# Optimization experiments

Hardware: AMD Instinct MI355X
Metric: run time of the kernel (lower is better)

## Reference

```python
import jax, jax.numpy as jnp
import numpy as np

B, S, E, H = 2, 2048, 1024, 16
D = E // H


def setup_inputs() -> dict:
    key = jax.random.key(0)
    ks = jax.random.split(key, 8)
    q = jax.random.normal(ks[0], (B, S, E), dtype=jnp.float32)
    k = jax.random.normal(ks[1], (B, S, E), dtype=jnp.float32)
    v = jax.random.normal(ks[2], (B, S, E), dtype=jnp.float32)
    mask = jax.random.randint(ks[3], (B, 1, 1, S), 0, 2, dtype=jnp.int32)
    sc = 1.0 / np.sqrt(E)
    W_qkv = jax.random.normal(ks[4], (3 * E, E), dtype=jnp.float32) * sc
    b_qkv = jnp.zeros((3 * E,), dtype=jnp.float32)
    W_out = jax.random.normal(ks[5], (E, E), dtype=jnp.float32) * sc
    b_out = jnp.zeros((E,), dtype=jnp.float32)
    return {"q": q, "k": k, "v": v, "mask": mask,
            "W_qkv": W_qkv, "b_qkv": b_qkv, "W_out": W_out, "b_out": b_out}


def reference(q, k, v, mask, W_qkv, b_qkv, W_out, b_out):
    # Fused qkv linear: q takes the Q-slice, k the K-slice, v the V-slice.
    qp = (q @ W_qkv[:E].T + b_qkv[:E]).reshape(B, S, H, D)
    kp = (k @ W_qkv[E:2 * E].T + b_qkv[E:2 * E]).reshape(B, S, H, D)
    vp = (v @ W_qkv[2 * E:].T + b_qkv[2 * E:]).reshape(B, S, H, D)
    # (B,H,S,S) scores -- NOTE: original module does NOT scale by sqrt(d)
    energy = jnp.einsum('nqhd,nkhd->nhqk', qp, kp)
    energy = jnp.where(mask == 0, jnp.float32(-1e20), energy)
    attention = jax.nn.softmax(energy, axis=-1)
    out = jnp.einsum('nhql,nlhd->nqhd', attention, vp).reshape(B, S, E)
    return out @ W_out.T + b_out
```

## Files before the change

kernel.cpp:

```cpp
#include <hip/hip_runtime.h>
#include <stdint.h>

constexpr int B_ = 2, S_ = 2048, E_ = 1024, H_ = 16, D_ = 64;
constexpr int M_ = B_ * S_;

typedef unsigned short u16;
typedef __attribute__((ext_vector_type(8))) short short8;
typedef __attribute__((ext_vector_type(4))) float f32x4;

__device__ __forceinline__ u16 f2bf(float f) {
  uint32_t u = __float_as_uint(f);
  return (u16)((u + 0x7FFFu + ((u >> 16) & 1u)) >> 16);
}
__device__ __forceinline__ void tsplit(float x, u16& hi, u16& lo) {
  const uint32_t u = __float_as_uint(x);
  hi = (u16)(u >> 16);
  const float hif = __uint_as_float(u & 0xFFFF0000u);
  lo = (u16)(__float_as_uint(x - hif) >> 16);
}

__device__ __forceinline__ void block_sync() {
  asm volatile("s_waitcnt lgkmcnt(0)" ::: "memory");
  __builtin_amdgcn_s_barrier();
}

__global__ __launch_bounds__(256) void split_f32_kernel(
    const float* __restrict__ src, u16* __restrict__ hi, u16* __restrict__ lo, int n4)
{
  const int i = blockIdx.x * 256 + threadIdx.x;
  if (i >= n4) return;
  const float4 x = ((const float4*)src)[i];
  ushort4 h, l;
  tsplit(x.x, h.x, l.x); tsplit(x.y, h.y, l.y);
  tsplit(x.z, h.z, l.z); tsplit(x.w, h.w, l.w);
  ((ushort4*)hi)[i] = h;
  ((ushort4*)lo)[i] = l;
}

__global__ __launch_bounds__(256) void mask_scan_kernel(
    const int* __restrict__ mask, int* __restrict__ opos, int* __restrict__ nk)
{
  __shared__ int tmp[256];
  __shared__ int coff;
  const int b = blockIdx.x, t = threadIdx.x;
  for (int c = t; c < S_; c += 256) opos[b * S_ + c] = 0;
  if (t == 0) coff = 0;
  __syncthreads();
  for (int c = 0; c < S_; c += 256) {
    const int m = (mask[b * S_ + c + t] != 0) ? 1 : 0;
    int x = m;
    tmp[t] = x;
    __syncthreads();
#pragma unroll
    for (int off = 1; off < 256; off <<= 1) {
      const int v = (t >= off) ? tmp[t - off] : 0;
      __syncthreads();
      x += v;
      tmp[t] = x;
      __syncthreads();
    }
    const int base = coff;
    if (m) opos[b * S_ + base + x - 1] = c + t;
    __syncthreads();
    if (t == 255) coff = base + x;
    __syncthreads();
  }
  if (t == 0) nk[b] = coff;
}

__global__ __launch_bounds__(256) void gemm_qkv_kernel(
    const float* __restrict__ q, const float* __restrict__ k, const float* __restrict__ v,
    const u16* __restrict__ WHi, const u16* __restrict__ WLo,
    const float* __restrict__ bias,
    const int* __restrict__ Opos, const int* __restrict__ NkArr,
    u16* __restrict__ QpHi, u16* __restrict__ QpLo,
    u16* __restrict__ KpHi, u16* __restrict__ KpLo,
    u16* __restrict__ Vp)
{
  __shared__ __align__(16) short smem[20480];
  short* Ah = smem;
  short* Al = smem + 5120;
  short* Bh = smem + 10240;
  short* Bl = smem + 15360;

  const int t = threadIdx.x;
  const int m0 = blockIdx.x * 128;
  const int n0g = blockIdx.y * 128;
  const int proj = n0g >> 10;
  const int nloc = n0g & (E_ - 1);
  const bool split = (proj < 2);
  const int bb = m0 >> 11, mloc = m0 & (S_ - 1);
  const int nkb = NkArr[bb];
  if (proj != 0 && mloc >= nkb) return;

  const float* A = (proj == 0) ? q : (proj == 1) ? k : v;

  const int w = t >> 6, lane = t & 63;
  const int g = lane >> 4, lc = lane & 15;
  const int wm = w & 1, wn = w >> 1;
  const int srow = t >> 1, sh = (t & 1) * 16;

  int arow;
  if (proj == 0) arow = m0 + srow;
  else arow = bb * S_ + (Opos[bb * S_ + mloc + srow] & (S_ - 1));
  const float* Ab = A + (size_t)arow * E_ + sh;
  const u16* Bhb = WHi + (size_t)(n0g + srow) * E_ + sh;
  const u16* Blb = WLo + (size_t)(n0g + srow) * E_ + sh;

  f32x4 acc[4][4];
#pragma unroll
  for (int i = 0; i < 4; ++i)
#pragma unroll
    for (int j = 0; j < 4; ++j) acc[i][j] = (f32x4){0.f, 0.f, 0.f, 0.f};

  float4 ar[4]; short8 br[2], cr[2];
#pragma unroll
  for (int i = 0; i < 4; ++i) ar[i] = *(const float4*)(Ab + 4 * i);
  br[0] = *(const short8*)(Bhb);     br[1] = *(const short8*)(Bhb + 8);
  if (split) { cr[0] = *(const short8*)(Blb); cr[1] = *(const short8*)(Blb + 8); }

  for (int k0 = 0; k0 < E_; k0 += 32) {
    __syncthreads();
    {
      ushort hh[16], ll[16];
#pragma unroll
      for (int i = 0; i < 4; ++i) {
        tsplit(ar[i].x, hh[4 * i + 0], ll[4 * i + 0]);
        tsplit(ar[i].y, hh[4 * i + 1], ll[4 * i + 1]);
        tsplit(ar[i].z, hh[4 * i + 2], ll[4 * i + 2]);
        tsplit(ar[i].w, hh[4 * i + 3], ll[4 * i + 3]);
      }
      *(short8*)&Ah[srow * 40 + sh]     = *(const short8*)&hh[0];
      *(short8*)&Ah[srow * 40 + sh + 8] = *(const short8*)&hh[8];
      if (split) {
        *(short8*)&Al[srow * 40 + sh]     = *(const short8*)&ll[0];
        *(short8*)&Al[srow * 40 + sh + 8] = *(const short8*)&ll[8];
      }
    }
    *(short8*)&Bh[srow * 40 + sh]     = br[0];
    *(short8*)&Bh[srow * 40 + sh + 8] = br[1];
    if (split) {
      *(short8*)&Bl[srow * 40 + sh]     = cr[0];
      *(short8*)&Bl[srow * 40 + sh + 8] = cr[1];
    }
    __syncthreads();
    if (k0 + 32 < E_) {
#pragma unroll
      for (int i = 0; i < 4; ++i) ar[i] = *(const float4*)(Ab + k0 + 32 + 4 * i);
      br[0] = *(const short8*)(Bhb + k0 + 32); br[1] = *(const short8*)(Bhb + k0 + 40);
      if (split) {
        cr[0] = *(const short8*)(Blb + k0 + 32); cr[1] = *(const short8*)(Blb + k0 + 40);
      }
    }

    short8 ah[4], al[4], bh[4], bl[4];
#pragma unroll
    for (int mt = 0; mt < 4; ++mt) {
      const int ro = (wm * 64 + mt * 16 + lc) * 40 + g * 8;
      ah[mt] = *(const short8*)&Ah[ro];
      if (split) al[mt] = *(const short8*)&Al[ro];
    }
#pragma unroll
    for (int nt = 0; nt < 4; ++nt) {
      const int ro = (wn * 64 + nt * 16 + lc) * 40 + g * 8;
      bh[nt] = *(const short8*)&Bh[ro];
      if (split) bl[nt] = *(const short8*)&Bl[ro];
    }
#pragma unroll
    for (int mt = 0; mt < 4; ++mt)
#pragma unroll
      for (int nt = 0; nt < 4; ++nt) {
        f32x4 a = acc[mt][nt];
        a = __builtin_amdgcn_mfma_f32_16x16x32_bf16(ah[mt], bh[nt], a, 0, 0, 0);
        if (split) {
          a = __builtin_amdgcn_mfma_f32_16x16x32_bf16(ah[mt], bl[nt], a, 0, 0, 0);
          a = __builtin_amdgcn_mfma_f32_16x16x32_bf16(al[mt], bh[nt], a, 0, 0, 0);
        }
        acc[mt][nt] = a;
      }
  }

  float bs[4];
#pragma unroll
  for (int nt = 0; nt < 4; ++nt) bs[nt] = bias[n0g + wn * 64 + nt * 16 + lc];

  if (proj < 2) {
    u16* Hi = (proj == 0) ? QpHi : KpHi;
    u16* Lo = (proj == 0) ? QpLo : KpLo;
    const int hwave = (nloc + wn * 64) >> 6;
    short* T = smem + w * 4608;
    const int srow_out = (proj == 0) ? ((m0 + wm * 64 + lane) & (S_ - 1))
                                     : (mloc + wm * 64 + lane);
    const size_t rowb = (((size_t)(bb * H_ + hwave)) * S_ + srow_out) * D_;
#pragma unroll
    for (int pass = 0; pass < 2; ++pass) {
      __syncthreads();
#pragma unroll
      for (int nt = 0; nt < 4; ++nt)
#pragma unroll
        for (int mt = 0; mt < 4; ++mt)
#pragma unroll
          for (int r = 0; r < 4; ++r) {
            const float val = acc[mt][nt][r] + bs[nt];
            const uint32_t u = __float_as_uint(val);
            u16 x;
            if (pass == 0) x = (u16)(u >> 16);
            else {
              const float hif = __uint_as_float(u & 0xFFFF0000u);
              x = (u16)(__float_as_uint(val - hif) >> 16);
            }
            T[(mt * 16 + g * 4 + r) * 72 + nt * 16 + lc] = (short)x;
          }
      __syncthreads();
      u16* dst = (pass == 0) ? Hi : Lo;
#pragma unroll
      for (int j = 0; j < 8; ++j)
        *(short8*)&dst[rowb + 8 * j] = *(const short8*)&T[lane * 72 + 8 * j];
    }
  } else {
#pragma unroll
    for (int mt = 0; mt < 4; ++mt) {
      const int jb = mloc + wm * 64 + mt * 16 + g * 4;
#pragma unroll
      for (int nt = 0; nt < 4; ++nt) {
        const int nE = nloc + wn * 64 + nt * 16 + lc;
        const int h = nE >> 6, d = nE & 63;
        const size_t rb = (((size_t)(bb * H_ + h)) * D_ + d) * S_;
#pragma unroll
        for (int r = 0; r < 4; ++r) {
          if (jb + r < nkb) Vp[rb + jb + r] = f2bf(acc[mt][nt][r] + bs[nt]);
        }
      }
    }
  }
}

__global__ __launch_bounds__(256, 4) void attn_mfma_kernel(
    const u16* __restrict__ QpHi, const u16* __restrict__ QpLo,
    const u16* __restrict__ KpHi, const u16* __restrict__ KpLo,
    const u16* __restrict__ Vp,
    const int* __restrict__ nkArr,
    u16* __restrict__ AOHi)
{
  __shared__ __align__(16) short sm[18432];
  short* Khi = sm;
  short* Klo = sm + 4608;
  short* Vt  = sm + 9216;
  short* Pb  = sm + 13824;

  const int t = threadIdx.x;
  const int w = t >> 6, lane = t & 63;
  const int g = lane >> 4, lc = lane & 15;
  const int bh = blockIdx.y;
  const int b = bh >> 4, hh = bh & 15;
  const int q0 = blockIdx.x * 64;
  const size_t hb = (size_t)bh * S_ * D_;
  const u16* QgH = QpHi + hb;
  const u16* QgL = QpLo + hb;
  const u16* KgH = KpHi + hb;
  const u16* KgL = KpLo + hb;
  const u16* Vg  = Vp + hb;
  short* Pw = Pb + w * 1152;

  const int nk = nkArr[b];
  const int kend = ((nk + 63) >> 6) << 6;

  short8 qh[2], ql[2];
  {
    const size_t base = (size_t)(q0 + 16 * w + lc) * D_ + 8 * g;
    qh[0] = *(const short8*)&QgH[base];
    qh[1] = *(const short8*)&QgH[base + 32];
    ql[0] = *(const short8*)&QgL[base];
    ql[1] = *(const short8*)&QgL[base + 32];
  }

  short8 ones8 = {0, 0, 0, 0, 0, 0, 0, 0};
  if (lc == 0) {
    const short o = (short)0x3F80;
    ones8 = (short8){o, o, o, o, o, o, o, o};
  }

  f32x4 O[4];
  f32x4 Ol = (f32x4){0.f, 0.f, 0.f, 0.f};
#pragma unroll
  for (int dt = 0; dt < 4; ++dt) O[dt] = (f32x4){0.f, 0.f, 0.f, 0.f};
  float mst[4] = {-INFINITY, -INFINITY, -INFINITY, -INFINITY};

  const int srow = t >> 2, sc16 = (t & 3) * 16;

  short8 kr[2], lr[2], vr[2];
  kr[0] = *(const short8*)&KgH[srow * D_ + sc16];
  kr[1] = *(const short8*)&KgH[srow * D_ + sc16 + 8];
  lr[0] = *(const short8*)&KgL[srow * D_ + sc16];
  lr[1] = *(const short8*)&KgL[srow * D_ + sc16 + 8];
  vr[0] = *(const short8*)&Vg[srow * S_ + sc16];
  vr[1] = *(const short8*)&Vg[srow * S_ + sc16 + 8];

  for (int kt = 0; kt < kend; kt += 64) {
    block_sync();
    *(short8*)&Khi[srow * 72 + sc16]     = kr[0];
    *(short8*)&Khi[srow * 72 + sc16 + 8] = kr[1];
    *(short8*)&Klo[srow * 72 + sc16]     = lr[0];
    *(short8*)&Klo[srow * 72 + sc16 + 8] = lr[1];
    *(short8*)&Vt[srow * 72 + sc16]      = vr[0];
    *(short8*)&Vt[srow * 72 + sc16 + 8]  = vr[1];
    block_sync();
    if (kt + 64 < kend) {
      const int kn = kt + 64;
      kr[0] = *(const short8*)&KgH[(kn + srow) * D_ + sc16];
      kr[1] = *(const short8*)&KgH[(kn + srow) * D_ + sc16 + 8];
      lr[0] = *(const short8*)&KgL[(kn + srow) * D_ + sc16];
      lr[1] = *(const short8*)&KgL[(kn + srow) * D_ + sc16 + 8];
      vr[0] = *(const short8*)&Vg[srow * S_ + kn + sc16];
      vr[1] = *(const short8*)&Vg[srow * S_ + kn + sc16 + 8];
    }

    f32x4 sc[4];
#pragma unroll
    for (int kt16 = 0; kt16 < 4; ++kt16) {
      const int ko = (16 * kt16 + lc) * 72 + 8 * g;
      const short8 kh0 = *(const short8*)&Khi[ko];
      const short8 kh1 = *(const short8*)&Khi[ko + 32];
      const short8 kl0 = *(const short8*)&Klo[ko];
      const short8 kl1 = *(const short8*)&Klo[ko + 32];
      f32x4 a = {0.f, 0.f, 0.f, 0.f};
      a = __builtin_amdgcn_mfma_f32_16x16x32_bf16(qh[0], kh0, a, 0, 0, 0);
      a = __builtin_amdgcn_mfma_f32_16x16x32_bf16(qh[1], kh1, a, 0, 0, 0);
      a = __builtin_amdgcn_mfma_f32_16x16x32_bf16(qh[0], kl0, a, 0, 0, 0);
      a = __builtin_amdgcn_mfma_f32_16x16x32_bf16(qh[1], kl1, a, 0, 0, 0);
      a = __builtin_amdgcn_mfma_f32_16x16x32_bf16(ql[0], kh0, a, 0, 0, 0);
      a = __builtin_amdgcn_mfma_f32_16x16x32_bf16(ql[1], kh1, a, 0, 0, 0);
      sc[kt16] = a;
    }

    if (kt + 64 > nk) {
#pragma unroll
      for (int kt16 = 0; kt16 < 4; ++kt16) {
        if (kt + 16 * kt16 + lc >= nk) {
          sc[kt16][0] = -1e20f; sc[kt16][1] = -1e20f;
          sc[kt16][2] = -1e20f; sc[kt16][3] = -1e20f;
        }
      }
    }

    float al[4];
#pragma unroll
    for (int r = 0; r < 4; ++r) {
      float vv = fmaxf(fmaxf(sc[0][r], sc[1][r]), fmaxf(sc[2][r], sc[3][r]));
      vv = fmaxf(vv, __shfl_xor(vv, 1));
      vv = fmaxf(vv, __shfl_xor(vv, 2));
      vv = fmaxf(vv, __shfl_xor(vv, 4));
      vv = fmaxf(vv, __shfl_xor(vv, 8));
      const float mn = fmaxf(mst[r], vv);
      al[r] = __expf(mst[r] - mn);
      mst[r] = mn;
    }
#pragma unroll
    for (int kt16 = 0; kt16 < 4; ++kt16) {
#pragma unroll
      for (int r = 0; r < 4; ++r)
        sc[kt16][r] = __expf(sc[kt16][r] - mst[r]);
    }
    const f32x4 alv = {al[0], al[1], al[2], al[3]};
    O[0] *= alv; O[1] *= alv; O[2] *= alv; O[3] *= alv;
    Ol *= alv;
#pragma unroll
    for (int kt16 = 0; kt16 < 4; ++kt16) {
#pragma unroll
      for (int r = 0; r < 4; ++r)
        Pw[(4 * g + r) * 72 + 16 * kt16 + lc] = (short)f2bf(sc[kt16][r]);
    }

    short8 pa[2];
    pa[0] = *(const short8*)&Pw[lc * 72 + 8 * g];
    pa[1] = *(const short8*)&Pw[lc * 72 + 32 + 8 * g];
    Ol = __builtin_amdgcn_mfma_f32_16x16x32_bf16(pa[0], ones8, Ol, 0, 0, 0);
    Ol = __builtin_amdgcn_mfma_f32_16x16x32_bf16(pa[1], ones8, Ol, 0, 0, 0);
#pragma unroll
    for (int dt = 0; dt < 4; ++dt) {
      const int vo = (16 * dt + lc) * 72 + 8 * g;
      const short8 vb0 = *(const short8*)&Vt[vo];
      const short8 vb1 = *(const short8*)&Vt[vo + 32];
      O[dt] = __builtin_amdgcn_mfma_f32_16x16x32_bf16(pa[0], vb0, O[dt], 0, 0, 0);
      O[dt] = __builtin_amdgcn_mfma_f32_16x16x32_bf16(pa[1], vb1, O[dt], 0, 0, 0);
    }
  }

#pragma unroll
  for (int r = 0; r < 4; ++r) {
    const float lv = __shfl(Ol[r], lane & 48);
    const float lir = 1.0f / lv;
    const int qrow = q0 + 16 * w + 4 * g + r;
    const size_t rowb = (size_t)(b * S_ + qrow) * E_ + hh * 64;
#pragma unroll
    for (int dt = 0; dt < 4; ++dt)
      AOHi[rowb + dt * 16 + lc] = f2bf(O[dt][r] * lir);
  }
}

__global__ __launch_bounds__(256) void gemm_out_kernel(
    const u16* __restrict__ AHi,
    const u16* __restrict__ WHi,
    const float* __restrict__ bias, float* __restrict__ out)
{
  __shared__ __align__(16) short smem[5120];
  short* Ah = smem;
  short* Bh = smem + 2560;

  const int t = threadIdx.x;
  const int m0 = blockIdx.x * 64;
  const int n0 = blockIdx.y * 64;
  const int w = t >> 6, lane = t & 63;
  const int g = lane >> 4, lc = lane & 15;
  const int wm = w & 1, wn = w >> 1;
  const int sr = t >> 2, sc = (t & 3) * 8;

  const u16* Ahb = AHi + (size_t)(m0 + sr) * E_ + sc;
  const u16* Bhb = WHi + (size_t)(n0 + sr) * E_ + sc;

  f32x4 acc[2][2];
#pragma unroll
  for (int i = 0; i < 2; ++i)
#pragma unroll
    for (int j = 0; j < 2; ++j) acc[i][j] = (f32x4){0.f, 0.f, 0.f, 0.f};

  short8 arP[2], brP[2];
  arP[0] = *(const short8*)(Ahb);
  arP[1] = *(const short8*)(Ahb + 32);
  brP[0] = *(const short8*)(Bhb);
  brP[1] = *(const short8*)(Bhb + 32);

#pragma unroll 2
  for (int k0 = 0; k0 < E_; k0 += 32) {
    const int p = (k0 >> 5) & 1;
    block_sync();
    *(short8*)&Ah[sr * 40 + sc] = arP[p];
    *(short8*)&Bh[sr * 40 + sc] = brP[p];
    block_sync();
    {
      const int kk = (k0 + 64) & (E_ - 1);
      arP[p] = *(const short8*)(Ahb + kk);
      brP[p] = *(const short8*)(Bhb + kk);
    }

    short8 ah[2], bh[2];
#pragma unroll
    for (int mt = 0; mt < 2; ++mt)
      ah[mt] = *(const short8*)&Ah[(wm * 32 + mt * 16 + lc) * 40 + g * 8];
#pragma unroll
    for (int nt = 0; nt < 2; ++nt)
      bh[nt] = *(const short8*)&Bh[(wn * 32 + nt * 16 + lc) * 40 + g * 8];
#pragma unroll
    for (int mt = 0; mt < 2; ++mt)
#pragma unroll
      for (int nt = 0; nt < 2; ++nt)
        acc[mt][nt] = __builtin_amdgcn_mfma_f32_16x16x32_bf16(ah[mt], bh[nt], acc[mt][nt], 0, 0, 0);
  }

  float bs[2];
#pragma unroll
  for (int nt = 0; nt < 2; ++nt) bs[nt] = bias[n0 + wn * 32 + nt * 16 + lc];
#pragma unroll
  for (int nt = 0; nt < 2; ++nt) {
    const int nc = n0 + wn * 32 + nt * 16 + lc;
#pragma unroll
    for (int mt = 0; mt < 2; ++mt) {
#pragma unroll
      for (int r = 0; r < 4; ++r) {
        const int mrow = m0 + wm * 32 + mt * 16 + g * 4 + r;
        out[(size_t)mrow * E_ + nc] = acc[mt][nt][r] + bs[nt];
      }
    }
  }
}

extern "C" void kernel_launch(void* const* d_in, const int* in_sizes, int n_in,
                              void* d_out, int out_size, void* d_ws, size_t ws_size,
                              hipStream_t stream) {
  const float* q    = (const float*)d_in[0];
  const float* k    = (const float*)d_in[1];
  const float* v    = (const float*)d_in[2];
  const int*   mask = (const int*)d_in[3];
  const float* Wqkv = (const float*)d_in[4];
  const float* bqkv = (const float*)d_in[5];
  const float* Wout = (const float*)d_in[6];
  const float* bout = (const float*)d_in[7];
  float* out = (float*)d_out;

  char* wsb = (char*)d_ws;
  u16* WqkvHi = (u16*)(wsb + 0);
  u16* WqkvLo = (u16*)(wsb + 6291456);
  u16* WoutHi = (u16*)(wsb + 12582912);
  int* Opos   = (int*)(wsb + 14680064);
  int* Nk     = (int*)(wsb + 14680064 + 16384);
  u16* WoutLo = (u16*)(wsb + 14680064);
  u16* QpHi   = (u16*)(wsb + 16777216);
  u16* QpLo   = (u16*)(wsb + 25165824);
  u16* KpHi   = (u16*)(wsb + 33554432);
  u16* KpLo   = (u16*)(wsb + 41943040);
  u16* Vp     = (u16*)(wsb + 50331648);
  u16* AOHi   = (u16*)(wsb + 58720256);

  hipLaunchKernelGGL(split_f32_kernel, dim3(3072), dim3(256), 0, stream,
                     Wqkv, WqkvHi, WqkvLo, 786432);
  hipLaunchKernelGGL(split_f32_kernel, dim3(1024), dim3(256), 0, stream,
                     Wout, WoutHi, WoutLo, 262144);
  hipLaunchKernelGGL(mask_scan_kernel, dim3(B_), dim3(256), 0, stream,
                     mask, Opos, Nk);
  hipMemsetAsync(Vp, 0, 8388608, stream);
  hipLaunchKernelGGL(gemm_qkv_kernel, dim3(M_ / 128, 24), dim3(256), 0, stream,
                     q, k, v, WqkvHi, WqkvLo, bqkv, Opos, Nk,
                     QpHi, QpLo, KpHi, KpLo, Vp);
  hipLaunchKernelGGL(attn_mfma_kernel, dim3(S_ / 64, B_ * H_), dim3(256), 0, stream,
                     QpHi, QpLo, KpHi, KpLo, Vp, Nk, AOHi);
  hipLaunchKernelGGL(gemm_out_kernel, dim3(M_ / 64, E_ / 64), dim3(256), 0, stream,
                     AOHi, WoutHi, bout, out);
}
```

Measured before the change: 294.0 us.

## Use direct global-to-LDS loads with XOR swizzle in QKV and output GEMMs

Weight tiles in the QKV GEMM are now loaded straight into LDS with global_load_lds and an XOR-swizzled unpadded layout, replacing the register-staged copies. The output GEMM also loads both operands this way, widens its N tile from 64 to 128, and drops its register double-buffering. The aim is to cut VGPR pressure and the LDS store instructions. The cost is that these loads are no longer overlapped with the previous iteration's MFMA work, so load latency may be exposed in the output GEMM, which now waits on a barrier every step.

Measured after the change: 266.4 us. 9.4% less time.

```diff
diff --git a/kernel.cpp b/kernel.cpp
--- a/kernel.cpp
+++ b/kernel.cpp
@@ -22,6 +22,12 @@
 __device__ __forceinline__ void block_sync() {
   asm volatile("s_waitcnt lgkmcnt(0)" ::: "memory");
   __builtin_amdgcn_s_barrier();
+}
+
+typedef const __attribute__((address_space(1))) unsigned int GU32;
+typedef __attribute__((address_space(3))) unsigned int LU32;
+__device__ __forceinline__ void gload16(const void* g, void* l) {
+  __builtin_amdgcn_global_load_lds((GU32*)g, (LU32*)l, 16, 0, 0);
 }
 
 __global__ __launch_bounds__(256) void split_f32_kernel(
@@ -77,11 +83,11 @@
     u16* __restrict__ KpHi, u16* __restrict__ KpLo,
     u16* __restrict__ Vp)
 {
-  __shared__ __align__(16) short smem[20480];
+  __shared__ __align__(16) short smem[18432];
   short* Ah = smem;
   short* Al = smem + 5120;
   short* Bh = smem + 10240;
-  short* Bl = smem + 15360;
+  short* Bl = smem + 14336;
 
   const int t = threadIdx.x;
   const int m0 = blockIdx.x * 128;
@@ -98,14 +104,12 @@
   const int w = t >> 6, lane = t & 63;
   const int g = lane >> 4, lc = lane & 15;
   const int wm = w & 1, wn = w >> 1;
-  const int srow = t >> 1, sh = (t & 1) * 16;
+  const int sra = t >> 1, sca = (t & 1) * 16;
 
   int arow;
-  if (proj == 0) arow = m0 + srow;
-  else arow = bb * S_ + (Opos[bb * S_ + mloc + srow] & (S_ - 1));
-  const float* Ab = A + (size_t)arow * E_ + sh;
-  const u16* Bhb = WHi + (size_t)(n0g + srow) * E_ + sh;
-  const u16* Blb = WLo + (size_t)(n0g + srow) * E_ + sh;
+  if (proj == 0) arow = m0 + sra;
+  else arow = bb * S_ + (Opos[bb * S_ + mloc + sra] & (S_ - 1));
+  const float* Ab = A + (size_t)arow * E_ + sca;
 
   f32x4 acc[4][4];
 #pragma unroll
@@ -113,45 +117,47 @@
 #pragma unroll
     for (int j = 0; j < 4; ++j) acc[i][j] = (f32x4){0.f, 0.f, 0.f, 0.f};
 
-  float4 ar[4]; short8 br[2], cr[2];
-#pragma unroll
-  for (int i = 0; i < 4; ++i) ar[i] = *(const float4*)(Ab + 4 * i);
-  br[0] = *(const short8*)(Bhb);     br[1] = *(const short8*)(Bhb + 8);
-  if (split) { cr[0] = *(const short8*)(Blb); cr[1] = *(const short8*)(Blb + 8); }
+  auto loadA = [&](float4* a, int kk) {
+#pragma unroll
+    for (int i = 0; i < 4; ++i) a[i] = *(const float4*)(Ab + kk + 4 * i);
+  };
+  auto writeA = [&](const float4* a) {
+    ushort hh[16], ll[16];
+#pragma unroll
+    for (int i = 0; i < 4; ++i) {
+      tsplit(a[i].x, hh[4 * i + 0], ll[4 * i + 0]);
+      tsplit(a[i].y, hh[4 * i + 1], ll[4 * i + 1]);
+      tsplit(a[i].z, hh[4 * i + 2], ll[4 * i + 2]);
+      tsplit(a[i].w, hh[4 * i + 3], ll[4 * i + 3]);
+    }
+    *(short8*)&Ah[sra * 40 + sca]     = *(const short8*)&hh[0];
+    *(short8*)&Ah[sra * 40 + sca + 8] = *(const short8*)&hh[8];
+    if (split) {
+      *(short8*)&Al[sra * 40 + sca]     = *(const short8*)&ll[0];
+      *(short8*)&Al[sra * 40 + sca + 8] = *(const short8*)&ll[8];
+    }
+  };
+  auto gloadB = [&](int k0) {
+#pragma unroll
+    for (int i = 0; i < 2; ++i) {
+      const int c = (w * 2 + i) * 64 + lane;
+      const int row = c >> 2;
+      const int sub = (c & 3) ^ ((row >> 1) & 3);
+      const size_t go = (size_t)(n0g + row) * E_ + k0 + sub * 8;
+      gload16(WHi + go, (char*)Bh + (w * 2 + i) * 1024);
+      if (split) gload16(WLo + go, (char*)Bl + (w * 2 + i) * 1024);
+    }
+  };
+
+  float4 ar[4];
+  loadA(ar, 0);
 
   for (int k0 = 0; k0 < E_; k0 += 32) {
     __syncthreads();
-    {
-      ushort hh[16], ll[16];
-#pragma unroll
-      for (int i = 0; i < 4; ++i) {
-        tsplit(ar[i].x, hh[4 * i + 0], ll[4 * i + 0]);
-        tsplit(ar[i].y, hh[4 * i + 1], ll[4 * i + 1]);
-        tsplit(ar[i].z, hh[4 * i + 2], ll[4 * i + 2]);
-        tsplit(ar[i].w, hh[4 * i + 3], ll[4 * i + 3]);
-      }
-      *(short8*)&Ah[srow * 40 + sh]     = *(const short8*)&hh[0];
-      *(short8*)&Ah[srow * 40 + sh + 8] = *(const short8*)&hh[8];
-      if (split) {
-        *(short8*)&Al[srow * 40 + sh]     = *(const short8*)&ll[0];
-        *(short8*)&Al[srow * 40 + sh + 8] = *(const short8*)&ll[8];
-      }
-    }
-    *(short8*)&Bh[srow * 40 + sh]     = br[0];
-    *(short8*)&Bh[srow * 40 + sh + 8] = br[1];
-    if (split) {
-      *(short8*)&Bl[srow * 40 + sh]     = cr[0];
-      *(short8*)&Bl[srow * 40 + sh + 8] = cr[1];
-    }
-    __syncthreads();
-    if (k0 + 32 < E_) {
-#pragma unroll
-      for (int i = 0; i < 4; ++i) ar[i] = *(const float4*)(Ab + k0 + 32 + 4 * i);
-      br[0] = *(const short8*)(Bhb + k0 + 32); br[1] = *(const short8*)(Bhb + k0 + 40);
-      if (split) {
-        cr[0] = *(const short8*)(Blb + k0 + 32); cr[1] = *(const short8*)(Blb + k0 + 40);
-      }
-    }
+    writeA(ar);
+    gloadB(k0);
+    __syncthreads();
+    if (k0 + 32 < E_) loadA(ar, k0 + 32);
 
     short8 ah[4], al[4], bh[4], bl[4];
 #pragma unroll
@@ -162,7 +168,8 @@
     }
 #pragma unroll
     for (int nt = 0; nt < 4; ++nt) {
-      const int ro = (wn * 64 + nt * 16 + lc) * 40 + g * 8;
+      const int row = wn * 64 + nt * 16 + lc;
+      const int ro = row * 32 + ((g ^ ((row >> 1) & 3)) * 8);
       bh[nt] = *(const short8*)&Bh[ro];
       if (split) bl[nt] = *(const short8*)&Bl[ro];
     }
@@ -403,66 +410,66 @@
     const u16* __restrict__ WHi,
     const float* __restrict__ bias, float* __restrict__ out)
 {
-  __shared__ __align__(16) short smem[5120];
+  __shared__ __align__(16) short smem[6144];
   short* Ah = smem;
-  short* Bh = smem + 2560;
+  short* Bh = smem + 2048;
 
   const int t = threadIdx.x;
   const int m0 = blockIdx.x * 64;
-  const int n0 = blockIdx.y * 64;
+  const int n0 = blockIdx.y * 128;
   const int w = t >> 6, lane = t & 63;
   const int g = lane >> 4, lc = lane & 15;
   const int wm = w & 1, wn = w >> 1;
-  const int sr = t >> 2, sc = (t & 3) * 8;
-
-  const u16* Ahb = AHi + (size_t)(m0 + sr) * E_ + sc;
-  const u16* Bhb = WHi + (size_t)(n0 + sr) * E_ + sc;
-
-  f32x4 acc[2][2];
+
+  f32x4 acc[2][4];
 #pragma unroll
   for (int i = 0; i < 2; ++i)
 #pragma unroll
-    for (int j = 0; j < 2; ++j) acc[i][j] = (f32x4){0.f, 0.f, 0.f, 0.f};
-
-  short8 arP[2], brP[2];
-  arP[0] = *(const short8*)(Ahb);
-  arP[1] = *(const short8*)(Ahb + 32);
-  brP[0] = *(const short8*)(Bhb);
-  brP[1] = *(const short8*)(Bhb + 32);
-
-#pragma unroll 2
+    for (int j = 0; j < 4; ++j) acc[i][j] = (f32x4){0.f, 0.f, 0.f, 0.f};
+
   for (int k0 = 0; k0 < E_; k0 += 32) {
-    const int p = (k0 >> 5) & 1;
-    block_sync();
-    *(short8*)&Ah[sr * 40 + sc] = arP[p];
-    *(short8*)&Bh[sr * 40 + sc] = brP[p];
-    block_sync();
     {
-      const int kk = (k0 + 64) & (E_ - 1);
-      arP[p] = *(const short8*)(Ahb + kk);
-      brP[p] = *(const short8*)(Bhb + kk);
-    }
-
-    short8 ah[2], bh[2];
+      const int cA = w * 64 + lane;
+      const int rowA = cA >> 2;
+      const int subA = (cA & 3) ^ ((rowA >> 1) & 3);
+      gload16(AHi + (size_t)(m0 + rowA) * E_ + k0 + subA * 8,
+              (char*)Ah + w * 1024);
+#pragma unroll
+      for (int i = 0; i < 2; ++i) {
+        const int c = (w * 2 + i) * 64 + lane;
+        const int row = c >> 2;
+        const int sub = (c & 3) ^ ((row >> 1) & 3);
+        gload16(WHi + (size_t)(n0 + row) * E_ + k0 + sub * 8,
+                (char*)Bh + (w * 2 + i) * 1024);
+      }
+    }
+    __syncthreads();
+
+    short8 ah[2], bh[4];
+#pragma unroll
+    for (int mt = 0; mt < 2; ++mt) {
+      const int row = wm * 32 + mt * 16 + lc;
+      ah[mt] = *(const short8*)&Ah[row * 32 + ((g ^ ((row >> 1) & 3)) * 8)];
+    }
+#pragma unroll
+    for (int nt = 0; nt < 4; ++nt) {
+      const int row = wn * 64 + nt * 16 + lc;
+      bh[nt] = *(const short8*)&Bh[row * 32 + ((g ^ ((row >> 1) & 3)) * 8)];
+    }
 #pragma unroll
     for (int mt = 0; mt < 2; ++mt)
-      ah[mt] = *(const short8*)&Ah[(wm * 32 + mt * 16 + lc) * 40 + g * 8];
-#pragma unroll
-    for (int nt = 0; nt < 2; ++nt)
-      bh[nt] = *(const short8*)&Bh[(wn * 32 + nt * 16 + lc) * 40 + g * 8];
-#pragma unroll
-    for (int mt = 0; mt < 2; ++mt)
-#pragma unroll
-      for (int nt = 0; nt < 2; ++nt)
+#pragma unroll
+      for (int nt = 0; nt < 4; ++nt)
         acc[mt][nt] = __builtin_amdgcn_mfma_f32_16x16x32_bf16(ah[mt], bh[nt], acc[mt][nt], 0, 0, 0);
-  }
-
-  float bs[2];
-#pragma unroll
-  for (int nt = 0; nt < 2; ++nt) bs[nt] = bias[n0 + wn * 32 + nt * 16 + lc];
-#pragma unroll
-  for (int nt = 0; nt < 2; ++nt) {
-    const int nc = n0 + wn * 32 + nt * 16 + lc;
+    __syncthreads();
+  }
+
+  float bs[4];
+#pragma unroll
+  for (int nt = 0; nt < 4; ++nt) bs[nt] = bias[n0 + wn * 64 + nt * 16 + lc];
+#pragma unroll
+  for (int nt = 0; nt < 4; ++nt) {
+    const int nc = n0 + wn * 64 + nt * 16 + lc;
 #pragma unroll
     for (int mt = 0; mt < 2; ++mt) {
 #pragma unroll
@@ -513,6 +520,6 @@
                      QpHi, QpLo, KpHi, KpLo, Vp);
   hipLaunchKernelGGL(attn_mfma_kernel, dim3(S_ / 64, B_ * H_), dim3(256), 0, stream,
                      QpHi, QpLo, KpHi, KpLo, Vp, Nk, AOHi);
-  hipLaunchKernelGGL(gemm_out_kernel, dim3(M_ / 64, E_ / 64), dim3(256), 0, stream,
+  hipLaunchKernelGGL(gemm_out_kernel, dim3(M_ / 64, E_ / 128), dim3(256), 0, stream,
                      AOHi, WoutHi, bout, out);
 }
```
